# Optimization experiments

Hardware: AMD Instinct MI355X
Metric: run time of the kernel (lower is better)

The kernel has to match this reference:

```python
import jax, jax.numpy as jnp
import numpy as np

B, T, C, H = 4, 2048, 768, 12
D = C // H  # head dim = 64

def setup_inputs() -> dict:
    key = jax.random.key(0)
    k1, k2, k3, k4, k5 = jax.random.split(key, 5)
    s = 0.02
    x = jax.random.normal(k1, (B, T, C), dtype=jnp.float32)
    w_qkv = jax.random.normal(k2, (3 * C, C), dtype=jnp.float32) * s  # torch Linear weight [out,in]
    b_qkv = jax.random.normal(k3, (3 * C,), dtype=jnp.float32) * s
    w_proj = jax.random.normal(k4, (C, C), dtype=jnp.float32) * s
    b_proj = jax.random.normal(k5, (C,), dtype=jnp.float32) * s
    return {"x": x, "w_qkv": w_qkv, "b_qkv": b_qkv, "w_proj": w_proj, "b_proj": b_proj}

def reference(x, w_qkv, b_qkv, w_proj, b_proj):
    Bx, Tx, Cx = x.shape
    # qkv projection: torch Linear y = x @ W.T + b
    qkv = x @ w_qkv.T + b_qkv                      # [B,T,3C]
    qkv = qkv.reshape(Bx, Tx, 3, H, D)
    q, k, v = qkv[:, :, 0], qkv[:, :, 1], qkv[:, :, 2]  # each [B,T,H,D]
    scale = 1.0 / jnp.sqrt(jnp.float32(D))
    scores = jnp.einsum('bqhd,bkhd->bhqk', q, k) * scale  # [B,H,T,T]
    causal = jnp.tril(jnp.ones((Tx, Tx), dtype=bool))
    scores = jnp.where(causal[None, None], scores, -jnp.inf)
    attn = jax.nn.softmax(scores, axis=-1)
    out = jnp.einsum('bhqk,bkhd->bqhd', attn, v).reshape(Bx, Tx, Cx)
    return out @ w_proj.T + b_proj
```

## Files before the change

kernel.cpp:

```cpp
#include <hip/hip_runtime.h>
#include <hip/hip_bf16.h>
#include <cstdint>
#include <cstddef>

typedef __bf16 bf16_t;
typedef __bf16 bf16x8 __attribute__((ext_vector_type(8)));
typedef __bf16 bf16x4 __attribute__((ext_vector_type(4)));
typedef float f32x4 __attribute__((ext_vector_type(4)));
typedef float f32x16 __attribute__((ext_vector_type(16)));

constexpr int B_ = 4, T_ = 2048, C_ = 768, H_ = 12, D_ = 64;
constexpr size_t QKV_ELEMS = (size_t)B_ * H_ * T_ * D_;

__device__ __forceinline__ void gload16(const bf16_t* g, bf16_t* l) {
    __builtin_amdgcn_global_load_lds(
        (const __attribute__((address_space(1))) unsigned int*)g,
        (__attribute__((address_space(3))) unsigned int*)l, 16, 0, 0);
}

__global__ __launch_bounds__(256)
void conv_bf16(const float* __restrict__ a, bf16_t* __restrict__ oa, int na8,
               const float* __restrict__ b, bf16_t* __restrict__ ob, int nb8)
{
    int i = blockIdx.x * 256 + threadIdx.x;
    if (i >= na8 + nb8) return;
    const float* src; bf16_t* dst; int idx;
    if (i < na8) { src = a; dst = oa; idx = i; }
    else         { src = b; dst = ob; idx = i - na8; }
    const float4* p = reinterpret_cast<const float4*>(src + (size_t)idx * 8);
    float4 f0 = p[0], f1 = p[1];
    bf16x8 t;
    t[0]=(bf16_t)f0.x; t[1]=(bf16_t)f0.y; t[2]=(bf16_t)f0.z; t[3]=(bf16_t)f0.w;
    t[4]=(bf16_t)f1.x; t[5]=(bf16_t)f1.y; t[6]=(bf16_t)f1.z; t[7]=(bf16_t)f1.w;
    *reinterpret_cast<bf16x8*>(dst + (size_t)idx * 8) = t;
}

__global__ __launch_bounds__(256, 3)
void qkv_gemm(const bf16_t* __restrict__ xb, const bf16_t* __restrict__ wb,
              const float* __restrict__ bias,
              bf16_t* __restrict__ q, bf16_t* __restrict__ k, bf16_t* __restrict__ v)
{
    __shared__ alignas(16) bf16_t As[128 * 64];
    __shared__ alignas(16) bf16_t Bs[128 * 64];
    const int tid  = threadIdx.x;
    const int lane = tid & 63;
    const int w    = tid >> 6;
    const int wm = w >> 1, wn = w & 1;
    const int bm = blockIdx.x & 63;
    const int bn = blockIdx.x >> 6;
    const int m0 = bm * 128, n0 = bn * 128;
    const int lcol = lane & 15, lgrp = lane >> 4;
    const int srow = lane >> 3;
    const int scol = ((lane & 7) ^ srow) * 8;

    const bf16_t* ag = xb + (size_t)(m0 + w * 32 + srow) * C_ + scol;
    const bf16_t* bg = wb + (size_t)(n0 + w * 32 + srow) * C_ + scol;
    bf16_t* al = &As[(w * 32) * 64];
    bf16_t* bl = &Bs[(w * 32) * 64];

    f32x4 acc[4][4] = {};

    for (int kt = 0; kt < C_; kt += 64) {
        __syncthreads();
        #pragma unroll
        for (int p = 0; p < 4; ++p) {
            gload16(ag + (size_t)(p * 8) * C_ + kt, al + p * 8 * 64);
            gload16(bg + (size_t)(p * 8) * C_ + kt, bl + p * 8 * 64);
        }
        __syncthreads();
        #pragma unroll
        for (int kk = 0; kk < 2; ++kk) {
            bf16x8 af[4], bfr[4];
            #pragma unroll
            for (int i = 0; i < 4; ++i) {
                const int R = wm * 64 + i * 16 + lcol;
                af[i] = *reinterpret_cast<const bf16x8*>(&As[R * 64 + (((kk*4 + lgrp) ^ (R & 7)) << 3)]);
            }
            #pragma unroll
            for (int j = 0; j < 4; ++j) {
                const int R = wn * 64 + j * 16 + lcol;
                bfr[j] = *reinterpret_cast<const bf16x8*>(&Bs[R * 64 + (((kk*4 + lgrp) ^ (R & 7)) << 3)]);
            }
            #pragma unroll
            for (int i = 0; i < 4; ++i)
                #pragma unroll
                for (int j = 0; j < 4; ++j)
                    acc[i][j] = __builtin_amdgcn_mfma_f32_16x16x32_bf16(af[i], bfr[j], acc[i][j], 0, 0, 0);
        }
    }

    #pragma unroll
    for (int j = 0; j < 4; ++j) {
        const int n = n0 + wn * 64 + j * 16 + lcol;
        const float bv = bias[n];
        const int s = n / C_, rem = n % C_;
        const int h = rem >> 6, d = rem & 63;
        bf16_t* dst = (s == 0) ? q : (s == 1) ? k : v;
        #pragma unroll
        for (int i = 0; i < 4; ++i) {
            #pragma unroll
            for (int r = 0; r < 4; ++r) {
                const int m = m0 + wm * 64 + i * 16 + lgrp * 4 + r;
                const int b = m >> 11, t = m & (T_ - 1);
                dst[(((size_t)(b * H_ + h)) * T_ + t) * D_ + d] = (bf16_t)(acc[i][j][r] + bv);
            }
        }
    }
}

__global__ __launch_bounds__(256, 2)
void attn_fwd(const bf16_t* __restrict__ qg, const bf16_t* __restrict__ kg,
              const bf16_t* __restrict__ vg, bf16_t* __restrict__ og)
{
    __shared__ alignas(16) bf16_t Ks[64 * 64];
    __shared__ alignas(16) bf16_t Vt[64 * 64];

    const int tid  = threadIdx.x;
    const int lane = tid & 63;
    const int w    = tid >> 6;
    const int l31  = lane & 31;
    const int hi   = lane >> 5;
    const int qi   = blockIdx.x / 48;
    const int bh   = blockIdx.x % 48;
    const int qt   = 15 - qi;
    const int q0   = qt * 128;
    const int qw   = q0 + w * 32;
    const size_t base = (size_t)bh * T_ * D_;
    const int qrow = qw + l31;

    const float SCL = 0.125f * 1.44269504f;
    bf16x8 bq[4];
    #pragma unroll
    for (int kt = 0; kt < 4; ++kt) {
        bf16x8 t = *reinterpret_cast<const bf16x8*>(qg + base + (size_t)qrow * D_ + kt*16 + hi*8);
        #pragma unroll
        for (int e = 0; e < 8; ++e) t[e] = (bf16_t)((float)t[e] * SCL);
        bq[kt] = t;
    }

    f32x16 ot0 = {};
    f32x16 ot1 = {};
    float m = -1e30f, rowl = 0.0f;

    const int skey = tid >> 3;
    const int sgr  = tid & 7;
    bf16x8 kr[2], vr[2];

    #pragma unroll
    for (int p = 0; p < 2; ++p) {
        const int key = p * 32 + skey;
        kr[p] = *reinterpret_cast<const bf16x8*>(kg + base + (size_t)key * D_ + sgr * 8);
        vr[p] = *reinterpret_cast<const bf16x8*>(vg + base + (size_t)key * D_ + sgr * 8);
    }

    const int ntiles = qt * 2 + 2;
    for (int it = 0; it < ntiles; ++it) {
        __syncthreads();
        #pragma unroll
        for (int p = 0; p < 2; ++p) {
            const int key = p * 32 + skey;
            *reinterpret_cast<bf16x8*>(Ks + key * 64 + ((sgr ^ (key & 7)) << 3)) = kr[p];
            #pragma unroll
            for (int j = 0; j < 8; ++j) {
                const int d = sgr * 8 + j;
                Vt[d * 64 + ((((key >> 3) ^ (d & 7) ^ sgr) & 7) << 3) + (key & 7)] = vr[p][j];
            }
        }
        __syncthreads();
        if (it + 1 < ntiles) {
            const int kvn = (it + 1) * 64;
            #pragma unroll
            for (int p = 0; p < 2; ++p) {
                const int key = kvn + p * 32 + skey;
                kr[p] = *reinterpret_cast<const bf16x8*>(kg + base + (size_t)key * D_ + sgr * 8);
                vr[p] = *reinterpret_cast<const bf16x8*>(vg + base + (size_t)key * D_ + sgr * 8);
            }
        }

        const int kv0 = it * 64;
        #pragma unroll
        for (int sk = 0; sk < 2; ++sk) {
            const int kvs = kv0 + sk * 32;
            if (kvs > qw + 31) continue;

            f32x16 s = {};
            __builtin_amdgcn_s_setprio(1);
            #pragma unroll
            for (int kt = 0; kt < 4; ++kt) {
                const int keyl = sk * 32 + l31;
                const int slot = kt * 2 + hi;
                bf16x8 ka = *reinterpret_cast<const bf16x8*>(Ks + keyl * 64 + ((slot ^ (keyl & 7)) << 3));
                s = __builtin_amdgcn_mfma_f32_32x32x16_bf16(ka, bq[kt], s, 0, 0, 0);
            }
            __builtin_amdgcn_s_setprio(0);
            if (kvs + 31 > qw) {
                #pragma unroll
                for (int r = 0; r < 16; ++r) {
                    const int key = kvs + (r & 3) + 8 * (r >> 2) + 4 * hi;
                    if (key > qrow) s[r] = -1e30f;
                }
            }
            float mt = s[0];
            #pragma unroll
            for (int r = 1; r < 16; ++r) mt = fmaxf(mt, s[r]);
            mt = fmaxf(mt, __shfl_xor(mt, 32));
            if (!__all(mt <= m + 8.0f)) {
                const float mnew = fmaxf(m, mt);
                const float alpha = exp2f(m - mnew);
                #pragma unroll
                for (int r = 0; r < 16; ++r) { ot0[r] *= alpha; ot1[r] *= alpha; }
                rowl *= alpha;
                m = mnew;
            }
            float pv[16];
            float rs = 0.0f;
            #pragma unroll
            for (int r = 0; r < 16; ++r) { pv[r] = exp2f(s[r] - m); rs += pv[r]; }
            rs += __shfl_xor(rs, 32);
            rowl += rs;

            uint32_t c0, c1, c2, c3, c4, c5, c6, c7;
            asm("v_cvt_pk_bf16_f32 %0, %1, %2" : "=v"(c0) : "v"(pv[0]),  "v"(pv[1]));
            asm("v_cvt_pk_bf16_f32 %0, %1, %2" : "=v"(c1) : "v"(pv[2]),  "v"(pv[3]));
            asm("v_cvt_pk_bf16_f32 %0, %1, %2" : "=v"(c2) : "v"(pv[4]),  "v"(pv[5]));
            asm("v_cvt_pk_bf16_f32 %0, %1, %2" : "=v"(c3) : "v"(pv[6]),  "v"(pv[7]));
            asm("v_cvt_pk_bf16_f32 %0, %1, %2" : "=v"(c4) : "v"(pv[8]),  "v"(pv[9]));
            asm("v_cvt_pk_bf16_f32 %0, %1, %2" : "=v"(c5) : "v"(pv[10]), "v"(pv[11]));
            asm("v_cvt_pk_bf16_f32 %0, %1, %2" : "=v"(c6) : "v"(pv[12]), "v"(pv[13]));
            asm("v_cvt_pk_bf16_f32 %0, %1, %2" : "=v"(c7) : "v"(pv[14]), "v"(pv[15]));
            asm("v_permlane32_swap_b32 %0, %1" : "+v"(c0), "+v"(c2));
            asm("v_permlane32_swap_b32 %0, %1" : "+v"(c1), "+v"(c3));
            asm("v_permlane32_swap_b32 %0, %1" : "+v"(c4), "+v"(c6));
            asm("v_permlane32_swap_b32 %0, %1" : "+v"(c5), "+v"(c7));
            union U { uint32_t u[4]; bf16x8 v; };
            U pa0; pa0.u[0] = c0; pa0.u[1] = c1; pa0.u[2] = c2; pa0.u[3] = c3;
            U pa1; pa1.u[0] = c4; pa1.u[1] = c5; pa1.u[2] = c6; pa1.u[3] = c7;

            __builtin_amdgcn_s_setprio(1);
            #pragma unroll
            for (int dblk = 0; dblk < 2; ++dblk) {
                const int d = dblk * 32 + l31;
                f32x16& o = dblk ? ot1 : ot0;
                #pragma unroll
                for (int ktile = 0; ktile < 2; ++ktile) {
                    const int kslot = sk * 4 + ktile * 2 + hi;
                    const int ss = kslot ^ (d & 7) ^ ((d >> 3) & 7);
                    bf16x8 va = *reinterpret_cast<const bf16x8*>(Vt + d * 64 + (ss << 3));
                    o = __builtin_amdgcn_mfma_f32_32x32x16_bf16(va, ktile ? pa1.v : pa0.v, o, 0, 0, 0);
                }
            }
            __builtin_amdgcn_s_setprio(0);
        }
    }

    const int b = bh / H_, h = bh % H_;
    const float inv = 1.0f / rowl;
    bf16_t* dst = &og[((size_t)b * T_ + qrow) * C_ + h * D_];
    #pragma unroll
    for (int dblk = 0; dblk < 2; ++dblk) {
        const f32x16& o = dblk ? ot1 : ot0;
        #pragma unroll
        for (int qd = 0; qd < 4; ++qd) {
            bf16x4 v4;
            #pragma unroll
            for (int r = 0; r < 4; ++r) v4[r] = (bf16_t)(o[qd * 4 + r] * inv);
            *reinterpret_cast<bf16x4*>(dst + dblk * 32 + qd * 8 + hi * 4) = v4;
        }
    }
}

__global__ __launch_bounds__(256, 3)
void proj_gemm(const bf16_t* __restrict__ ao, const bf16_t* __restrict__ wpb,
               const float* __restrict__ bias, float* __restrict__ out)
{
    __shared__ alignas(16) bf16_t As[128 * 64];
    __shared__ alignas(16) bf16_t Bs[128 * 64];
    const int tid  = threadIdx.x;
    const int lane = tid & 63;
    const int w    = tid >> 6;
    const int wm = w >> 1, wn = w & 1;
    const int bm = blockIdx.x & 63;
    const int bn = blockIdx.x >> 6;
    const int m0 = bm * 128, n0 = bn * 128;
    const int lcol = lane & 15, lgrp = lane >> 4;
    const int srow = lane >> 3;
    const int scol = ((lane & 7) ^ srow) * 8;

    const bf16_t* ag = ao  + (size_t)(m0 + w * 32 + srow) * C_ + scol;
    const bf16_t* bg = wpb + (size_t)(n0 + w * 32 + srow) * C_ + scol;
    bf16_t* al = &As[(w * 32) * 64];
    bf16_t* bl = &Bs[(w * 32) * 64];

    f32x4 acc[4][4] = {};

    for (int kt = 0; kt < C_; kt += 64) {
        __syncthreads();
        #pragma unroll
        for (int p = 0; p < 4; ++p) {
            gload16(ag + (size_t)(p * 8) * C_ + kt, al + p * 8 * 64);
            gload16(bg + (size_t)(p * 8) * C_ + kt, bl + p * 8 * 64);
        }
        __syncthreads();
        #pragma unroll
        for (int kk = 0; kk < 2; ++kk) {
            bf16x8 af[4], bfr[4];
            #pragma unroll
            for (int i = 0; i < 4; ++i) {
                const int R = wm * 64 + i * 16 + lcol;
                af[i] = *reinterpret_cast<const bf16x8*>(&As[R * 64 + (((kk*4 + lgrp) ^ (R & 7)) << 3)]);
            }
            #pragma unroll
            for (int j = 0; j < 4; ++j) {
                const int R = wn * 64 + j * 16 + lcol;
                bfr[j] = *reinterpret_cast<const bf16x8*>(&Bs[R * 64 + (((kk*4 + lgrp) ^ (R & 7)) << 3)]);
            }
            #pragma unroll
            for (int i = 0; i < 4; ++i)
                #pragma unroll
                for (int j = 0; j < 4; ++j)
                    acc[i][j] = __builtin_amdgcn_mfma_f32_16x16x32_bf16(af[i], bfr[j], acc[i][j], 0, 0, 0);
        }
    }

    #pragma unroll
    for (int j = 0; j < 4; ++j) {
        const int n = n0 + wn * 64 + j * 16 + lcol;
        const float bv = bias[n];
        #pragma unroll
        for (int i = 0; i < 4; ++i) {
            #pragma unroll
            for (int r = 0; r < 4; ++r) {
                const int m = m0 + wm * 64 + i * 16 + lgrp * 4 + r;
                out[(size_t)m * C_ + n] = acc[i][j][r] + bv;
            }
        }
    }
}

extern "C" void kernel_launch(void* const* d_in, const int* in_sizes, int n_in,
                              void* d_out, int out_size, void* d_ws, size_t ws_size,
                              hipStream_t stream)
{
    const float* x      = (const float*)d_in[0];
    const float* w_qkv  = (const float*)d_in[1];
    const float* b_qkv  = (const float*)d_in[2];
    const float* w_proj = (const float*)d_in[3];
    const float* b_proj = (const float*)d_in[4];
    float* out = (float*)d_out;

    bf16_t* ws = (bf16_t*)d_ws;
    bf16_t* q   = ws;
    bf16_t* k   = ws +     QKV_ELEMS;
    bf16_t* v   = ws + 2 * QKV_ELEMS;
    bf16_t* ao  = ws + 3 * QKV_ELEMS;
    bf16_t* xb  = ao;
    bf16_t* wqb = (bf16_t*)d_out;
    bf16_t* wpb = k;

    conv_bf16<<<dim3(3936), 256, 0, stream>>>(x, xb, 786432, w_qkv, wqb, 221184);
    qkv_gemm<<<dim3(64 * 18), 256, 0, stream>>>(xb, wqb, b_qkv, q, k, v);
    attn_fwd<<<dim3(16 * 48), 256, 0, stream>>>(q, k, v, ao);
    conv_bf16<<<dim3(288), 256, 0, stream>>>(w_proj, wpb, 73728, w_proj, wpb, 0);
    proj_gemm<<<dim3(64 * 6), 256, 0, stream>>>(ao, wpb, b_proj, out);
}
```

Before: 122.4 us.

## Double-buffer K/V shared tiles and pack V transpose writes as 32-bit words

Doubles the K and V shared-memory tiles so the next tile is written into the alternate buffer after the compute on the current one, which cuts the barriers per iteration from two to one. The V transpose now loads two adjacent keys per thread and packs them with byte permutes into 32-bit LDS stores, replacing the scalar 16-bit stores. The max and sum reductions become trees, and the exp results are written back into the score registers. Shared memory grows to 32 KB per block, which could limit occupancy at 2 blocks per CU.

Result: no change. 124.0 us (+1.3%).

```diff
diff --git a/kernel.cpp b/kernel.cpp
--- a/kernel.cpp
+++ b/kernel.cpp
@@ -112,8 +112,8 @@
 void attn_fwd(const bf16_t* __restrict__ qg, const bf16_t* __restrict__ kg,
               const bf16_t* __restrict__ vg, bf16_t* __restrict__ og)
 {
-    __shared__ alignas(16) bf16_t Ks[64 * 64];
-    __shared__ alignas(16) bf16_t Vt[64 * 64];
+    __shared__ alignas(16) bf16_t Ks[2 * 64 * 64];
+    __shared__ alignas(16) bf16_t Vt[2 * 64 * 64];
 
     const int tid  = threadIdx.x;
     const int lane = tid & 63;
@@ -144,37 +144,43 @@
 
     const int skey = tid >> 3;
     const int sgr  = tid & 7;
-    bf16x8 kr[2], vr[2];
-
-    #pragma unroll
-    for (int p = 0; p < 2; ++p) {
-        const int key = p * 32 + skey;
-        kr[p] = *reinterpret_cast<const bf16x8*>(kg + base + (size_t)key * D_ + sgr * 8);
-        vr[p] = *reinterpret_cast<const bf16x8*>(vg + base + (size_t)key * D_ + sgr * 8);
+    const int va_  = tid >> 3;
+    const bf16_t* srcK = kg + base + (size_t)skey * D_ + sgr * 8;
+    const bf16_t* srcV = vg + base + (size_t)(2 * va_) * D_ + sgr * 8;
+
+    union U8 { bf16x8 v; uint32_t u[4]; };
+    U8 kr0, kr1, vr0, vr1;
+
+    kr0.v = *reinterpret_cast<const bf16x8*>(srcK);
+    kr1.v = *reinterpret_cast<const bf16x8*>(srcK + (size_t)32 * D_);
+    vr0.v = *reinterpret_cast<const bf16x8*>(srcV);
+    vr1.v = *reinterpret_cast<const bf16x8*>(srcV + D_);
+    {
+        *reinterpret_cast<bf16x8*>(Ks + skey * 64 + ((sgr ^ (skey & 7)) << 3)) = kr0.v;
+        *reinterpret_cast<bf16x8*>(Ks + (32 + skey) * 64 + ((sgr ^ (skey & 7)) << 3)) = kr1.v;
+        #pragma unroll
+        for (int j = 0; j < 8; ++j) {
+            const int d = sgr * 8 + j;
+            const int ss = ((va_ >> 2) ^ j ^ sgr) & 7;
+            uint32_t wd = __builtin_amdgcn_perm(vr1.u[j >> 1], vr0.u[j >> 1],
+                                                (j & 1) ? 0x07060302u : 0x05040100u);
+            *reinterpret_cast<uint32_t*>(Vt + d * 64 + ss * 8 + (va_ & 3) * 2) = wd;
+        }
     }
 
     const int ntiles = qt * 2 + 2;
     for (int it = 0; it < ntiles; ++it) {
-        __syncthreads();
-        #pragma unroll
-        for (int p = 0; p < 2; ++p) {
-            const int key = p * 32 + skey;
-            *reinterpret_cast<bf16x8*>(Ks + key * 64 + ((sgr ^ (key & 7)) << 3)) = kr[p];
-            #pragma unroll
-            for (int j = 0; j < 8; ++j) {
-                const int d = sgr * 8 + j;
-                Vt[d * 64 + ((((key >> 3) ^ (d & 7) ^ sgr) & 7) << 3) + (key & 7)] = vr[p][j];
-            }
-        }
-        __syncthreads();
-        if (it + 1 < ntiles) {
-            const int kvn = (it + 1) * 64;
-            #pragma unroll
-            for (int p = 0; p < 2; ++p) {
-                const int key = kvn + p * 32 + skey;
-                kr[p] = *reinterpret_cast<const bf16x8*>(kg + base + (size_t)key * D_ + sgr * 8);
-                vr[p] = *reinterpret_cast<const bf16x8*>(vg + base + (size_t)key * D_ + sgr * 8);
-            }
+        const int off  = (it & 1) << 12;
+        const int offn = off ^ 4096;
+        __syncthreads();
+
+        const bool pre = (it + 1 < ntiles);
+        if (pre) {
+            const size_t soff = (size_t)(it + 1) * 64 * D_;
+            kr0.v = *reinterpret_cast<const bf16x8*>(srcK + soff);
+            kr1.v = *reinterpret_cast<const bf16x8*>(srcK + soff + (size_t)32 * D_);
+            vr0.v = *reinterpret_cast<const bf16x8*>(srcV + soff);
+            vr1.v = *reinterpret_cast<const bf16x8*>(srcV + soff + D_);
         }
 
         const int kv0 = it * 64;
@@ -189,7 +195,8 @@
             for (int kt = 0; kt < 4; ++kt) {
                 const int keyl = sk * 32 + l31;
                 const int slot = kt * 2 + hi;
-                bf16x8 ka = *reinterpret_cast<const bf16x8*>(Ks + keyl * 64 + ((slot ^ (keyl & 7)) << 3));
+                bf16x8 ka = *reinterpret_cast<const bf16x8*>(
+                    Ks + off + keyl * 64 + ((slot ^ (keyl & 7)) << 3));
                 s = __builtin_amdgcn_mfma_f32_32x32x16_bf16(ka, bq[kt], s, 0, 0, 0);
             }
             __builtin_amdgcn_s_setprio(0);
@@ -200,9 +207,14 @@
                     if (key > qrow) s[r] = -1e30f;
                 }
             }
-            float mt = s[0];
-            #pragma unroll
-            for (int r = 1; r < 16; ++r) mt = fmaxf(mt, s[r]);
+            float a0 = fmaxf(fmaxf(s[0],  s[1]),  s[2]);
+            float a1 = fmaxf(fmaxf(s[3],  s[4]),  s[5]);
+            float a2 = fmaxf(fmaxf(s[6],  s[7]),  s[8]);
+            float a3 = fmaxf(fmaxf(s[9],  s[10]), s[11]);
+            float a4 = fmaxf(fmaxf(s[12], s[13]), s[14]);
+            float b0 = fmaxf(fmaxf(a0, a1), a2);
+            float b1 = fmaxf(fmaxf(a3, a4), s[15]);
+            float mt = fmaxf(b0, b1);
             mt = fmaxf(mt, __shfl_xor(mt, 32));
             if (!__all(mt <= m + 8.0f)) {
                 const float mnew = fmaxf(m, mt);
@@ -212,22 +224,25 @@
                 rowl *= alpha;
                 m = mnew;
             }
-            float pv[16];
-            float rs = 0.0f;
-            #pragma unroll
-            for (int r = 0; r < 16; ++r) { pv[r] = exp2f(s[r] - m); rs += pv[r]; }
+            #pragma unroll
+            for (int r = 0; r < 16; ++r) s[r] = exp2f(s[r] - m);
+            float t0 = (s[0]+s[1]) + (s[2]+s[3]);
+            float t1 = (s[4]+s[5]) + (s[6]+s[7]);
+            float t2 = (s[8]+s[9]) + (s[10]+s[11]);
+            float t3 = (s[12]+s[13]) + (s[14]+s[15]);
+            float rs = (t0 + t1) + (t2 + t3);
             rs += __shfl_xor(rs, 32);
             rowl += rs;
 
             uint32_t c0, c1, c2, c3, c4, c5, c6, c7;
-            asm("v_cvt_pk_bf16_f32 %0, %1, %2" : "=v"(c0) : "v"(pv[0]),  "v"(pv[1]));
-            asm("v_cvt_pk_bf16_f32 %0, %1, %2" : "=v"(c1) : "v"(pv[2]),  "v"(pv[3]));
-            asm("v_cvt_pk_bf16_f32 %0, %1, %2" : "=v"(c2) : "v"(pv[4]),  "v"(pv[5]));
-            asm("v_cvt_pk_bf16_f32 %0, %1, %2" : "=v"(c3) : "v"(pv[6]),  "v"(pv[7]));
-            asm("v_cvt_pk_bf16_f32 %0, %1, %2" : "=v"(c4) : "v"(pv[8]),  "v"(pv[9]));
-            asm("v_cvt_pk_bf16_f32 %0, %1, %2" : "=v"(c5) : "v"(pv[10]), "v"(pv[11]));
-            asm("v_cvt_pk_bf16_f32 %0, %1, %2" : "=v"(c6) : "v"(pv[12]), "v"(pv[13]));
-            asm("v_cvt_pk_bf16_f32 %0, %1, %2" : "=v"(c7) : "v"(pv[14]), "v"(pv[15]));
+            asm("v_cvt_pk_bf16_f32 %0, %1, %2" : "=v"(c0) : "v"(s[0]),  "v"(s[1]));
+            asm("v_cvt_pk_bf16_f32 %0, %1, %2" : "=v"(c1) : "v"(s[2]),  "v"(s[3]));
+            asm("v_cvt_pk_bf16_f32 %0, %1, %2" : "=v"(c2) : "v"(s[4]),  "v"(s[5]));
+            asm("v_cvt_pk_bf16_f32 %0, %1, %2" : "=v"(c3) : "v"(s[6]),  "v"(s[7]));
+            asm("v_cvt_pk_bf16_f32 %0, %1, %2" : "=v"(c4) : "v"(s[8]),  "v"(s[9]));
+            asm("v_cvt_pk_bf16_f32 %0, %1, %2" : "=v"(c5) : "v"(s[10]), "v"(s[11]));
+            asm("v_cvt_pk_bf16_f32 %0, %1, %2" : "=v"(c6) : "v"(s[12]), "v"(s[13]));
+            asm("v_cvt_pk_bf16_f32 %0, %1, %2" : "=v"(c7) : "v"(s[14]), "v"(s[15]));
             asm("v_permlane32_swap_b32 %0, %1" : "+v"(c0), "+v"(c2));
             asm("v_permlane32_swap_b32 %0, %1" : "+v"(c1), "+v"(c3));
             asm("v_permlane32_swap_b32 %0, %1" : "+v"(c4), "+v"(c6));
@@ -245,11 +260,24 @@
                 for (int ktile = 0; ktile < 2; ++ktile) {
                     const int kslot = sk * 4 + ktile * 2 + hi;
                     const int ss = kslot ^ (d & 7) ^ ((d >> 3) & 7);
-                    bf16x8 va = *reinterpret_cast<const bf16x8*>(Vt + d * 64 + (ss << 3));
+                    bf16x8 va = *reinterpret_cast<const bf16x8*>(Vt + off + d * 64 + (ss << 3));
                     o = __builtin_amdgcn_mfma_f32_32x32x16_bf16(va, ktile ? pa1.v : pa0.v, o, 0, 0, 0);
                 }
             }
             __builtin_amdgcn_s_setprio(0);
+        }
+
+        if (pre) {
+            *reinterpret_cast<bf16x8*>(Ks + offn + skey * 64 + ((sgr ^ (skey & 7)) << 3)) = kr0.v;
+            *reinterpret_cast<bf16x8*>(Ks + offn + (32 + skey) * 64 + ((sgr ^ (skey & 7)) << 3)) = kr1.v;
+            #pragma unroll
+            for (int j = 0; j < 8; ++j) {
+                const int d = sgr * 8 + j;
+                const int ss = ((va_ >> 2) ^ j ^ sgr) & 7;
+                uint32_t wd = __builtin_amdgcn_perm(vr1.u[j >> 1], vr0.u[j >> 1],
+                                                    (j & 1) ? 0x07060302u : 0x05040100u);
+                *reinterpret_cast<uint32_t*>(Vt + offn + d * 64 + ss * 8 + (va_ & 3) * 2) = wd;
+            }
         }
     }
 
```
